# Kernel optimization log

Hardware: AMD Instinct MI355X
Metric: run time of the kernel (lower is better)

## Reference

```python
import jax, jax.numpy as jnp
import numpy as np

NUM_HEADS = 8
LN_EPS = 1e-8


def setup_inputs() -> dict:
    key = jax.random.key(0)
    ks = jax.random.split(key, 10)
    B, Sq, Sk, D, U = 8, 1024, 1024, 512, 512
    s = 1.0 / np.sqrt(D)
    return {
        "queries": jax.random.normal(ks[0], (B, Sq, D), jnp.float32),
        "keys": jax.random.normal(ks[1], (B, Sk, D), jnp.float32),
        "Wq": jax.random.normal(ks[2], (D, U), jnp.float32) * s,
        "bq": jnp.zeros((U,), jnp.float32),
        "Wk": jax.random.normal(ks[3], (D, U), jnp.float32) * s,
        "bk": jnp.zeros((U,), jnp.float32),
        "Wv": jax.random.normal(ks[4], (D, U), jnp.float32) * s,
        "bv": jnp.zeros((U,), jnp.float32),
        "gamma": jnp.ones((U,), jnp.float32),
        "beta": jnp.zeros((U,), jnp.float32),
    }


def reference(queries, keys, Wq, bq, Wk, bk, Wv, bv, gamma, beta):
    H = NUM_HEADS
    B, Sq, _ = queries.shape
    Sk = keys.shape[1]
    U = Wq.shape[1]
    Dh = U // H

    # ReLU-activated Q/K/V projections
    Q = jax.nn.relu(queries @ Wq + bq)   # [B,Sq,U]
    K = jax.nn.relu(keys @ Wk + bk)      # [B,Sk,U]
    V = jax.nn.relu(keys @ Wv + bv)      # [B,Sk,U]

    # split_heads: concat(split(x, H, -1), 0) == head-major [H,B,S,Dh]
    Qh = Q.reshape(B, Sq, H, Dh).transpose(2, 0, 1, 3)
    Kh = K.reshape(B, Sk, H, Dh).transpose(2, 0, 1, 3)
    Vh = V.reshape(B, Sk, H, Dh).transpose(2, 0, 1, 3)

    scores = jnp.einsum('hbqd,hbkd->hbqk', Qh, Kh) / jnp.sqrt(
        jnp.asarray(Dh, scores_dtype := Qh.dtype))
    attn = jax.nn.softmax(scores, axis=-1)

    # post-softmax query mask: zero rows where sum(|q|)==0 ([B,Sq,1] bcast)
    qmask = (jnp.sum(jnp.abs(queries), axis=-1, keepdims=True) > 0)
    attn = attn * qmask.astype(attn.dtype)[None]  # [1,B,Sq,1] -> [H,B,Sq,Sk]

    out = jnp.einsum('hbqk,hbkd->hbqd', attn, Vh)  # [H,B,Sq,Dh]
    # merge_heads: inverse of split_heads
    out = out.transpose(1, 2, 0, 3).reshape(B, Sq, U)

    out = out + queries  # residual

    # LayerNorm over last axis (keras default), eps=1e-8
    mu = jnp.mean(out, axis=-1, keepdims=True)
    var = jnp.mean(jnp.square(out - mu), axis=-1, keepdims=True)
    return gamma * (out - mu) * jax.lax.rsqrt(var + LN_EPS) + beta
```

## Files before the change

kernel.cpp:

```cpp
#include <hip/hip_runtime.h>
#include <stdint.h>

#define ROWS 8192
#define UDIM 512
#define SEQ  1024
#define NH   8
#define DH   64
#define SCALE 0.125f
#define LOG2E 1.44269504f
#define SC_Q (SCALE * LOG2E)

typedef unsigned short u16;
typedef __bf16 bf16_t;
typedef bf16_t bf16x8 __attribute__((ext_vector_type(8)));
typedef float f32x4 __attribute__((ext_vector_type(4)));

__device__ __forceinline__ u16 f2bf(float f) {
    union { float f; uint32_t u; } v; v.f = f;
    uint32_t r = v.u + 0x7FFFu + ((v.u >> 16) & 1u);
    return (u16)(r >> 16);
}

__device__ __forceinline__ uint32_t pk_bf16(float a, float b) {
#if __has_builtin(__builtin_amdgcn_cvt_pk_bf16_f32)
    typedef __bf16 bf16x2_t __attribute__((ext_vector_type(2)));
    bf16x2_t r = __builtin_amdgcn_cvt_pk_bf16_f32(a, b);
    union { bf16x2_t v; uint32_t u; } c; c.v = r;
    return c.u;
#else
    return (uint32_t)f2bf(a) | ((uint32_t)f2bf(b) << 16);
#endif
}

__device__ __forceinline__ void async_ld16(u16* lds, const u16* g) {
    __builtin_amdgcn_global_load_lds((const __attribute__((address_space(1))) void*)g,
                                     (__attribute__((address_space(3))) void*)lds, 16, 0, 0);
}

__global__ void convqk_kernel(const float* __restrict__ q, const float* __restrict__ k,
                              u16* __restrict__ qb, u16* __restrict__ kb) {
    int w = threadIdx.x >> 6, lane = threadIdx.x & 63;
    int row = blockIdx.x * 4 + w;
    const float* src = (blockIdx.y == 0) ? q : k;
    u16* dst = (blockIdx.y == 0) ? qb : kb;
    const float4* s4 = (const float4*)(src + (size_t)row * UDIM);
    ushort4* o4 = (ushort4*)(dst + (size_t)row * UDIM);
    for (int j = 0; j < 2; j++) {
        float4 v = s4[j * 64 + lane];
        ushort4 b;
        b.x = f2bf(v.x); b.y = f2bf(v.y); b.z = f2bf(v.z); b.w = f2bf(v.w);
        o4[j * 64 + lane] = b;
    }
}

__global__ void transposeW_kernel(const float* __restrict__ Wq, const float* __restrict__ Wk,
                                  const float* __restrict__ Wv, u16* __restrict__ Wqt,
                                  u16* __restrict__ Wkt, u16* __restrict__ Wvt) {
    const float* in = (blockIdx.z == 0) ? Wq : (blockIdx.z == 1) ? Wk : Wv;
    u16* out = (blockIdx.z == 0) ? Wqt : (blockIdx.z == 1) ? Wkt : Wvt;
    __shared__ float tile[32][33];
    int k0 = blockIdx.y * 32, n0 = blockIdx.x * 32;
    int tx = threadIdx.x & 31, ty = threadIdx.x >> 5;
    for (int r = ty; r < 32; r += 8)
        tile[r][tx] = in[(size_t)(k0 + r) * UDIM + n0 + tx];
    __syncthreads();
    for (int r = ty; r < 32; r += 8)
        out[(size_t)(n0 + r) * UDIM + k0 + tx] = f2bf(tile[tx][r]);
}

#define CPAD 136
__global__ __launch_bounds__(256, 3) void proj_kernel(
    const u16* __restrict__ qb, const u16* __restrict__ kb,
    const u16* __restrict__ Wqt, const u16* __restrict__ Wkt, const u16* __restrict__ Wvt,
    const float* __restrict__ bq, const float* __restrict__ bk, const float* __restrict__ bv,
    u16* __restrict__ Qp, u16* __restrict__ Kp, u16* __restrict__ Vtp)
{
    const int z = blockIdx.z;
    const u16* A = (z == 0) ? qb : kb;
    const u16* W = (z == 0) ? Wqt : (z == 1) ? Wkt : Wvt;
    const float* bias = (z == 0) ? bq : (z == 1) ? bk : bv;

    __shared__ u16 smem[128 * CPAD];
    u16* c_s = smem;

    const int t = threadIdx.x;
    const int lane = t & 63, w = t >> 6;
    const int quad = lane >> 4, l15 = lane & 15;
    const int m0 = blockIdx.x * 128;
    const int n0 = blockIdx.y * 128;

    const int r0 = t >> 2;
    const int s0 = ((t & 3) ^ ((r0 >> 1) & 3)) * 8;
    const u16* Ag0 = &A[(size_t)(m0 + r0) * 512 + s0];
    const u16* Ag1 = Ag0 + (size_t)64 * 512;
    const u16* Wg0 = &W[(size_t)(n0 + r0) * 512 + s0];
    const u16* Wg1 = Wg0 + (size_t)64 * 512;
    u16* al0[2] = { &smem[0 + t * 8],     &smem[4096 + t * 8] };
    u16* al1[2] = { &smem[0 + (t + 256) * 8], &smem[4096 + (t + 256) * 8] };
    u16* bl0[2] = { &smem[8192 + t * 8],      &smem[12288 + t * 8] };
    u16* bl1[2] = { &smem[8192 + (t + 256) * 8], &smem[12288 + (t + 256) * 8] };

    int aoff[2], boff[8];
    for (int mi = 0; mi < 2; mi++) {
        int row = w * 32 + mi * 16 + l15;
        aoff[mi] = row * 32 + (quad ^ ((row >> 1) & 3)) * 8;
    }
    for (int ni = 0; ni < 8; ni++) {
        int row = ni * 16 + l15;
        boff[ni] = row * 32 + (quad ^ ((row >> 1) & 3)) * 8;
    }

    f32x4 acc[2][8];
    for (int mi = 0; mi < 2; mi++)
        for (int ni = 0; ni < 8; ni++)
            acc[mi][ni] = (f32x4){0.f, 0.f, 0.f, 0.f};

    async_ld16(al0[0], Ag0);  async_ld16(al1[0], Ag1);
    async_ld16(bl0[0], Wg0);  async_ld16(bl1[0], Wg1);
    Ag0 += 32; Ag1 += 32; Wg0 += 32; Wg1 += 32;
    __syncthreads();

    for (int kt = 0; kt < 16; kt++) {
        const int cur = kt & 1, nxt = cur ^ 1;
        if (kt < 15) {
            async_ld16(al0[nxt], Ag0);  async_ld16(al1[nxt], Ag1);
            async_ld16(bl0[nxt], Wg0);  async_ld16(bl1[nxt], Wg1);
            Ag0 += 32; Ag1 += 32; Wg0 += 32; Wg1 += 32;
        }
        const int ab = cur ? 4096 : 0, bb = cur ? 12288 : 8192;
        bf16x8 af[2], bf[8];
        for (int mi = 0; mi < 2; mi++) af[mi] = *(const bf16x8*)&smem[ab + aoff[mi]];
        for (int ni = 0; ni < 8; ni++) bf[ni] = *(const bf16x8*)&smem[bb + boff[ni]];
        for (int mi = 0; mi < 2; mi++)
            for (int ni = 0; ni < 8; ni++)
                acc[mi][ni] = __builtin_amdgcn_mfma_f32_16x16x32_bf16(af[mi], bf[ni], acc[mi][ni], 0, 0, 0);
        __syncthreads();
    }

    const float qscale = (z == 0) ? SC_Q : 1.f;
    float bvl[8];
    for (int ni = 0; ni < 8; ni++) bvl[ni] = bias[n0 + ni * 16 + l15];
    for (int mi = 0; mi < 2; mi++)
        for (int ni = 0; ni < 8; ni++)
            for (int r = 0; r < 4; r++)
                acc[mi][ni][r] = fmaxf(acc[mi][ni][r] + bvl[ni], 0.f) * qscale;

    if (z < 2) {
        for (int mi = 0; mi < 2; mi++)
            for (int ni = 0; ni < 8; ni++)
                for (int r = 0; r < 4; r++)
                    c_s[(w * 32 + mi * 16 + quad * 4 + r) * CPAD + ni * 16 + l15] =
                        f2bf(acc[mi][ni][r]);
        __syncthreads();
        u16* outp = (z == 0) ? Qp : Kp;
        for (int j = 0; j < 8; j++) {
            int c = t + j * 256;
            int mrow = c >> 4, col8 = c & 15;
            uint4 d = *(const uint4*)&c_s[mrow * CPAD + col8 * 8];
            *(uint4*)&outp[(size_t)(m0 + mrow) * 512 + n0 + col8 * 8] = d;
        }
    } else {
        for (int mi = 0; mi < 2; mi++)
            for (int ni = 0; ni < 8; ni++) {
                uint2 pk;
                pk.x = pk_bf16(acc[mi][ni][0], acc[mi][ni][1]);
                pk.y = pk_bf16(acc[mi][ni][2], acc[mi][ni][3]);
                *(uint2*)&c_s[(ni * 16 + l15) * CPAD + w * 32 + mi * 16 + quad * 4] = pk;
            }
        __syncthreads();
        const int bb2 = m0 >> 10, sk0 = m0 & 1023;
        for (int j = 0; j < 8; j++) {
            int c = t + j * 256;
            int nrow = c >> 4, col8 = c & 15;
            uint4 d = *(const uint4*)&c_s[nrow * CPAD + col8 * 8];
            *(uint4*)&Vtp[(size_t)(bb2 * 512 + n0 + nrow) * 1024 + sk0 + col8 * 8] = d;
        }
    }
}

__global__ __launch_bounds__(256, 4) void attn_kernel(
    const u16* __restrict__ Qb, const u16* __restrict__ Kb, const u16* __restrict__ Vt,
    float* __restrict__ O)
{
    __shared__ u16 k_s[2][64 * 64];
    __shared__ u16 v_s[2][64 * 64];
    __shared__ u16 p_s[64 * 64];

    const int t = threadIdx.x, lane = t & 63, w = t >> 6;
    const int quad = lane >> 4, l15 = lane & 15;
    const int fid = blockIdx.x;
    const int xcd = fid & 7, j = fid >> 3;
    const int hb = xcd * 8 + (j & 7);
    const int qt = j >> 3;
    const int h = hb & 7, b = hb >> 3;
    const int q0 = qt * 64;

    const int r0 = t >> 3;
    const int s0 = ((t & 7) ^ (r0 & 7)) * 8;
    const u16* kg0 = &Kb[(size_t)(b * 1024 + r0) * 512 + h * 64 + s0];
    const u16* kg1 = kg0 + (size_t)32 * 512;
    const u16* vg0 = &Vt[(size_t)(b * 512 + h * 64 + r0) * 1024 + s0];
    const u16* vg1 = vg0 + (size_t)32 * 1024;
    u16* kd0[2] = { &k_s[0][t * 8], &k_s[1][t * 8] };
    u16* kd1[2] = { &k_s[0][(t + 256) * 8], &k_s[1][(t + 256) * 8] };
    u16* vd0[2] = { &v_s[0][t * 8], &v_s[1][t * 8] };
    u16* vd1[2] = { &v_s[0][(t + 256) * 8], &v_s[1][(t + 256) * 8] };

    const int prow = w * 16 + l15;
    bf16x8 bqf[2];
    {
        int qrow = b * 1024 + q0 + prow;
        for (int kk = 0; kk < 2; kk++)
            bqf[kk] = *(const bf16x8*)&Qb[(size_t)qrow * 512 + h * 64 + kk * 32 + quad * 8];
    }

    int koff[4][2], pwoff[4], proff[2];
    for (int mi = 0; mi < 4; mi++) {
        int row = mi * 16 + l15;
        koff[mi][0] = row * 64 + (quad ^ (row & 7)) * 8;
        koff[mi][1] = row * 64 + ((4 + quad) ^ (row & 7)) * 8;
    }
    for (int mi = 0; mi < 4; mi++)
        pwoff[mi] = prow * 64 + ((mi * 2 + (quad >> 1)) ^ (prow & 7)) * 8 + (quad & 1) * 4;
    for (int kk = 0; kk < 2; kk++)
        proff[kk] = prow * 64 + ((kk * 4 + quad) ^ (prow & 7)) * 8;

    float l_lane = 0.f;
    f32x4 o_acc[4];
    for (int mi = 0; mi < 4; mi++) o_acc[mi] = (f32x4){0.f, 0.f, 0.f, 0.f};

    async_ld16(kd0[0], kg0);  async_ld16(kd1[0], kg1);
    async_ld16(vd0[0], vg0);  async_ld16(vd1[0], vg1);
    kg0 += (size_t)64 * 512; kg1 += (size_t)64 * 512;
    vg0 += 64; vg1 += 64;
    __syncthreads();

    for (int it = 0; it < 16; it++) {
        const int cur = it & 1, nxt = cur ^ 1;

        if (it < 15) {
            async_ld16(kd0[nxt], kg0);  async_ld16(kd1[nxt], kg1);
            async_ld16(vd0[nxt], vg0);  async_ld16(vd1[nxt], vg1);
            kg0 += (size_t)64 * 512; kg1 += (size_t)64 * 512;
            vg0 += 64; vg1 += 64;
        }

        bf16x8 ak[4][2];
        for (int mi = 0; mi < 4; mi++) {
            ak[mi][0] = *(const bf16x8*)&k_s[cur][koff[mi][0]];
            ak[mi][1] = *(const bf16x8*)&k_s[cur][koff[mi][1]];
        }
        bf16x8 av[2][4];
        for (int kk = 0; kk < 2; kk++)
            for (int mi = 0; mi < 4; mi++)
                av[kk][mi] = *(const bf16x8*)&v_s[cur][koff[mi][kk]];

        f32x4 st[4];
        for (int mi = 0; mi < 4; mi++) {
            f32x4 a = (f32x4){0.f, 0.f, 0.f, 0.f};
            a = __builtin_amdgcn_mfma_f32_16x16x32_bf16(ak[mi][0], bqf[0], a, 0, 0, 0);
            a = __builtin_amdgcn_mfma_f32_16x16x32_bf16(ak[mi][1], bqf[1], a, 0, 0, 0);
            st[mi] = a;
        }
        for (int mi = 0; mi < 4; mi++) {
            float p0 = exp2f(st[mi][0]);
            float p1 = exp2f(st[mi][1]);
            float p2 = exp2f(st[mi][2]);
            float p3 = exp2f(st[mi][3]);
            l_lane += (p0 + p1) + (p2 + p3);
            uint2 pk;
            pk.x = pk_bf16(p0, p1);
            pk.y = pk_bf16(p2, p3);
            *(uint2*)&p_s[pwoff[mi]] = pk;
        }

        __syncthreads();

        for (int kk = 0; kk < 2; kk++) {
            bf16x8 bp = *(const bf16x8*)&p_s[proff[kk]];
            for (int mi = 0; mi < 4; mi++)
                o_acc[mi] = __builtin_amdgcn_mfma_f32_16x16x32_bf16(av[kk][mi], bp, o_acc[mi], 0, 0, 0);
        }

        if (it < 15)
            __syncthreads();
    }

    float l = l_lane;
    l += __shfl_xor(l, 16, 64);
    l += __shfl_xor(l, 32, 64);
    float inv = 1.f / l;
    int gq = q0 + prow;
    for (int mi = 0; mi < 4; mi++) {
        float4 o;
        o.x = o_acc[mi][0] * inv;
        o.y = o_acc[mi][1] * inv;
        o.z = o_acc[mi][2] * inv;
        o.w = o_acc[mi][3] * inv;
        *(float4*)&O[(size_t)(b * 1024 + gq) * 512 + h * 64 + mi * 16 + quad * 4] = o;
    }
}

__global__ void ln_kernel(const float* __restrict__ O, const float* __restrict__ q,
                          const float* __restrict__ gamma, const float* __restrict__ beta,
                          float* __restrict__ out)
{
    int w = threadIdx.x >> 6, lane = threadIdx.x & 63;
    int row = blockIdx.x * 4 + w;
    const float4* O4 = (const float4*)(O + (size_t)row * UDIM);
    const float4* q4 = (const float4*)(q + (size_t)row * UDIM);
    float4* o4 = (float4*)(out + (size_t)row * UDIM);

    float4 qq[2], oo[2];
    float am = 0.f;
    for (int j = 0; j < 2; j++) {
        qq[j] = q4[j * 64 + lane];
        oo[j] = O4[j * 64 + lane];
        am += fabsf(qq[j].x) + fabsf(qq[j].y) + fabsf(qq[j].z) + fabsf(qq[j].w);
    }
    for (int off = 32; off; off >>= 1) am += __shfl_xor(am, off, 64);
    float mask = (am > 0.f) ? 1.f : 0.f;

    float4 x[2];
    float s = 0.f, ss = 0.f;
    for (int j = 0; j < 2; j++) {
        float4 v;
        v.x = oo[j].x * mask + qq[j].x;
        v.y = oo[j].y * mask + qq[j].y;
        v.z = oo[j].z * mask + qq[j].z;
        v.w = oo[j].w * mask + qq[j].w;
        x[j] = v;
        s += v.x + v.y + v.z + v.w;
        ss += v.x * v.x + v.y * v.y + v.z * v.z + v.w * v.w;
    }
    for (int off = 32; off; off >>= 1) {
        s += __shfl_xor(s, off, 64);
        ss += __shfl_xor(ss, off, 64);
    }
    float mu = s * (1.f / 512.f);
    float var = ss * (1.f / 512.f) - mu * mu;
    float rs = rsqrtf(var + 1e-8f);
    for (int j = 0; j < 2; j++) {
        float4 g = ((const float4*)gamma)[j * 64 + lane];
        float4 bb = ((const float4*)beta)[j * 64 + lane];
        float4 v;
        v.x = g.x * (x[j].x - mu) * rs + bb.x;
        v.y = g.y * (x[j].y - mu) * rs + bb.y;
        v.z = g.z * (x[j].z - mu) * rs + bb.z;
        v.w = g.w * (x[j].w - mu) * rs + bb.w;
        o4[j * 64 + lane] = v;
    }
}

extern "C" void kernel_launch(void* const* d_in, const int* in_sizes, int n_in,
                              void* d_out, int out_size, void* d_ws, size_t ws_size,
                              hipStream_t stream)
{
    const float* queries = (const float*)d_in[0];
    const float* keys    = (const float*)d_in[1];
    const float* Wq      = (const float*)d_in[2];
    const float* bq      = (const float*)d_in[3];
    const float* Wk      = (const float*)d_in[4];
    const float* bk      = (const float*)d_in[5];
    const float* Wv      = (const float*)d_in[6];
    const float* bv      = (const float*)d_in[7];
    const float* gamma   = (const float*)d_in[8];
    const float* beta    = (const float*)d_in[9];
    float* out = (float*)d_out;

    char* ws = (char*)d_ws;
    size_t off = 0;
    auto alloc = [&](size_t bytes) {
        void* p = ws + off;
        off += (bytes + 255) & ~(size_t)255;
        return p;
    };
    u16* qb   = (u16*)alloc((size_t)ROWS * UDIM * 2);
    u16* kb   = (u16*)alloc((size_t)ROWS * UDIM * 2);
    u16* Wqt  = (u16*)alloc((size_t)UDIM * UDIM * 2);
    u16* Wkt  = (u16*)alloc((size_t)UDIM * UDIM * 2);
    u16* Wvt  = (u16*)alloc((size_t)UDIM * UDIM * 2);
    u16* Qp   = (u16*)alloc((size_t)ROWS * UDIM * 2);
    u16* Kp   = (u16*)alloc((size_t)ROWS * UDIM * 2);
    u16* Vtp  = (u16*)alloc((size_t)ROWS * UDIM * 2);
    float* Of = (float*)alloc((size_t)ROWS * UDIM * 4);

    convqk_kernel<<<dim3(ROWS / 4, 2), 256, 0, stream>>>(queries, keys, qb, kb);
    transposeW_kernel<<<dim3(16, 16, 3), 256, 0, stream>>>(Wq, Wk, Wv, Wqt, Wkt, Wvt);
    proj_kernel<<<dim3(64, 4, 3), 256, 0, stream>>>(qb, kb, Wqt, Wkt, Wvt, bq, bk, bv, Qp, Kp, Vtp);
    attn_kernel<<<1024, 256, 0, stream>>>(Qp, Kp, Vtp, Of);
    ln_kernel<<<ROWS / 4, 256, 0, stream>>>(Of, queries, gamma, beta, out);
}
```

Measured before the change: 160.5 us.

## Switch attention to 32x32x16 MFMA tiles and emit bf16 attention output

Reworks the attention kernel so each wave computes a 32x32 score and output tile with mfma_f32_32x32x16_bf16 instead of sets of 16x16x32 tiles. Each wave now covers only half of the 64-key block, so the row-sum l is combined across waves through LDS. The normalized output is staged through LDS and written as bf16 rather than fp32, halving the intermediate write and the LayerNorm read. The cost is lower output precision before the residual and LayerNorm, plus extra synchronization in the epilogue.

```diff
diff --git a/kernel.cpp b/kernel.cpp
--- a/kernel.cpp
+++ b/kernel.cpp
@@ -14,11 +14,17 @@
 typedef __bf16 bf16_t;
 typedef bf16_t bf16x8 __attribute__((ext_vector_type(8)));
 typedef float f32x4 __attribute__((ext_vector_type(4)));
+typedef float f32x16 __attribute__((ext_vector_type(16)));
 
 __device__ __forceinline__ u16 f2bf(float f) {
     union { float f; uint32_t u; } v; v.f = f;
     uint32_t r = v.u + 0x7FFFu + ((v.u >> 16) & 1u);
     return (u16)(r >> 16);
+}
+
+__device__ __forceinline__ float bf2f(u16 b) {
+    union { uint32_t u; float f; } v; v.u = ((uint32_t)b) << 16;
+    return v.f;
 }
 
 __device__ __forceinline__ uint32_t pk_bf16(float a, float b) {
@@ -180,14 +186,16 @@
 
 __global__ __launch_bounds__(256, 4) void attn_kernel(
     const u16* __restrict__ Qb, const u16* __restrict__ Kb, const u16* __restrict__ Vt,
-    float* __restrict__ O)
+    u16* __restrict__ Obf)
 {
     __shared__ u16 k_s[2][64 * 64];
     __shared__ u16 v_s[2][64 * 64];
     __shared__ u16 p_s[64 * 64];
 
     const int t = threadIdx.x, lane = t & 63, w = t >> 6;
-    const int quad = lane >> 4, l15 = lane & 15;
+    const int l31 = lane & 31, half = lane >> 5;
+    const int wh = w & 1;
+    const int wq = w >> 1;
     const int fid = blockIdx.x;
     const int xcd = fid & 7, j = fid >> 3;
     const int hb = xcd * 8 + (j & 7);
@@ -206,28 +214,29 @@
     u16* vd0[2] = { &v_s[0][t * 8], &v_s[1][t * 8] };
     u16* vd1[2] = { &v_s[0][(t + 256) * 8], &v_s[1][(t + 256) * 8] };
 
-    const int prow = w * 16 + l15;
-    bf16x8 bqf[2];
+    bf16x8 bqf[4];
     {
-        int qrow = b * 1024 + q0 + prow;
-        for (int kk = 0; kk < 2; kk++)
-            bqf[kk] = *(const bf16x8*)&Qb[(size_t)qrow * 512 + h * 64 + kk * 32 + quad * 8];
-    }
-
-    int koff[4][2], pwoff[4], proff[2];
-    for (int mi = 0; mi < 4; mi++) {
-        int row = mi * 16 + l15;
-        koff[mi][0] = row * 64 + (quad ^ (row & 7)) * 8;
-        koff[mi][1] = row * 64 + ((4 + quad) ^ (row & 7)) * 8;
-    }
-    for (int mi = 0; mi < 4; mi++)
-        pwoff[mi] = prow * 64 + ((mi * 2 + (quad >> 1)) ^ (prow & 7)) * 8 + (quad & 1) * 4;
-    for (int kk = 0; kk < 2; kk++)
-        proff[kk] = prow * 64 + ((kk * 4 + quad) ^ (prow & 7)) * 8;
+        int qrow = b * 1024 + q0 + 32 * wq + l31;
+        for (int tk = 0; tk < 4; tk++)
+            bqf[tk] = *(const bf16x8*)&Qb[(size_t)qrow * 512 + h * 64 + tk * 16 + half * 8];
+    }
+
+    int koff[4];
+    {
+        int row = 32 * wh + l31;
+        for (int tk = 0; tk < 4; tk++)
+            koff[tk] = row * 64 + (((2 * tk + half) ^ (row & 7))) * 8;
+    }
+    const int prow = 32 * wq + l31;
+    int pwoff[4], proff[4];
+    for (int g = 0; g < 4; g++)
+        pwoff[g] = prow * 64 + ((4 * wh + g) ^ (prow & 7)) * 8 + half * 4;
+    for (int tk = 0; tk < 4; tk++)
+        proff[tk] = prow * 64 + ((2 * tk + half) ^ (prow & 7)) * 8;
 
     float l_lane = 0.f;
-    f32x4 o_acc[4];
-    for (int mi = 0; mi < 4; mi++) o_acc[mi] = (f32x4){0.f, 0.f, 0.f, 0.f};
+    f32x16 o_acc = (f32x16){0.f,0.f,0.f,0.f,0.f,0.f,0.f,0.f,
+                            0.f,0.f,0.f,0.f,0.f,0.f,0.f,0.f};
 
     async_ld16(kd0[0], kg0);  async_ld16(kd1[0], kg1);
     async_ld16(vd0[0], vg0);  async_ld16(vd1[0], vg1);
@@ -245,79 +254,86 @@
             vg0 += 64; vg1 += 64;
         }
 
-        bf16x8 ak[4][2];
-        for (int mi = 0; mi < 4; mi++) {
-            ak[mi][0] = *(const bf16x8*)&k_s[cur][koff[mi][0]];
-            ak[mi][1] = *(const bf16x8*)&k_s[cur][koff[mi][1]];
-        }
-        bf16x8 av[2][4];
-        for (int kk = 0; kk < 2; kk++)
-            for (int mi = 0; mi < 4; mi++)
-                av[kk][mi] = *(const bf16x8*)&v_s[cur][koff[mi][kk]];
-
-        f32x4 st[4];
-        for (int mi = 0; mi < 4; mi++) {
-            f32x4 a = (f32x4){0.f, 0.f, 0.f, 0.f};
-            a = __builtin_amdgcn_mfma_f32_16x16x32_bf16(ak[mi][0], bqf[0], a, 0, 0, 0);
-            a = __builtin_amdgcn_mfma_f32_16x16x32_bf16(ak[mi][1], bqf[1], a, 0, 0, 0);
-            st[mi] = a;
-        }
-        for (int mi = 0; mi < 4; mi++) {
-            float p0 = exp2f(st[mi][0]);
-            float p1 = exp2f(st[mi][1]);
-            float p2 = exp2f(st[mi][2]);
-            float p3 = exp2f(st[mi][3]);
+        bf16x8 ak[4], av[4];
+        for (int tk = 0; tk < 4; tk++) {
+            ak[tk] = *(const bf16x8*)&k_s[cur][koff[tk]];
+            av[tk] = *(const bf16x8*)&v_s[cur][koff[tk]];
+        }
+
+        f32x16 st = (f32x16){0.f,0.f,0.f,0.f,0.f,0.f,0.f,0.f,
+                             0.f,0.f,0.f,0.f,0.f,0.f,0.f,0.f};
+        for (int tk = 0; tk < 4; tk++)
+            st = __builtin_amdgcn_mfma_f32_32x32x16_bf16(ak[tk], bqf[tk], st, 0, 0, 0);
+
+        for (int g = 0; g < 4; g++) {
+            float p0 = exp2f(st[4 * g + 0]);
+            float p1 = exp2f(st[4 * g + 1]);
+            float p2 = exp2f(st[4 * g + 2]);
+            float p3 = exp2f(st[4 * g + 3]);
             l_lane += (p0 + p1) + (p2 + p3);
             uint2 pk;
             pk.x = pk_bf16(p0, p1);
             pk.y = pk_bf16(p2, p3);
-            *(uint2*)&p_s[pwoff[mi]] = pk;
+            *(uint2*)&p_s[pwoff[g]] = pk;
         }
 
         __syncthreads();
 
-        for (int kk = 0; kk < 2; kk++) {
-            bf16x8 bp = *(const bf16x8*)&p_s[proff[kk]];
-            for (int mi = 0; mi < 4; mi++)
-                o_acc[mi] = __builtin_amdgcn_mfma_f32_16x16x32_bf16(av[kk][mi], bp, o_acc[mi], 0, 0, 0);
+        for (int tk = 0; tk < 4; tk++) {
+            bf16x8 bp = *(const bf16x8*)&p_s[proff[tk]];
+            o_acc = __builtin_amdgcn_mfma_f32_32x32x16_bf16(av[tk], bp, o_acc, 0, 0, 0);
         }
 
         if (it < 15)
             __syncthreads();
     }
 
-    float l = l_lane;
-    l += __shfl_xor(l, 16, 64);
-    l += __shfl_xor(l, 32, 64);
-    float inv = 1.f / l;
-    int gq = q0 + prow;
-    for (int mi = 0; mi < 4; mi++) {
-        float4 o;
-        o.x = o_acc[mi][0] * inv;
-        o.y = o_acc[mi][1] * inv;
-        o.z = o_acc[mi][2] * inv;
-        o.w = o_acc[mi][3] * inv;
-        *(float4*)&O[(size_t)(b * 1024 + gq) * 512 + h * 64 + mi * 16 + quad * 4] = o;
-    }
-}
-
-__global__ void ln_kernel(const float* __restrict__ O, const float* __restrict__ q,
+    __syncthreads();
+    float l2 = l_lane + __shfl_xor(l_lane, 32, 64);
+    float* lbuf = (float*)&k_s[0][0];
+    if (lane < 32) lbuf[w * 32 + l31] = l2;
+    __syncthreads();
+    float ltot = lbuf[w * 32 + l31] + lbuf[(w ^ 1) * 32 + l31];
+    float inv = 1.f / ltot;
+
+    for (int g = 0; g < 4; g++) {
+        uint2 pk;
+        pk.x = pk_bf16(o_acc[4 * g + 0] * inv, o_acc[4 * g + 1] * inv);
+        pk.y = pk_bf16(o_acc[4 * g + 2] * inv, o_acc[4 * g + 3] * inv);
+        *(uint2*)&p_s[pwoff[g]] = pk;
+    }
+    __syncthreads();
+    for (int rnd = 0; rnd < 2; rnd++) {
+        int c = t + rnd * 256;
+        int row = c >> 3, slot = c & 7;
+        int phys = slot ^ (row & 7);
+        uint4 d4 = *(const uint4*)&p_s[row * 64 + phys * 8];
+        *(uint4*)&Obf[(size_t)(b * 1024 + q0 + row) * 512 + h * 64 + slot * 8] = d4;
+    }
+}
+
+__global__ void ln_kernel(const u16* __restrict__ O, const float* __restrict__ q,
                           const float* __restrict__ gamma, const float* __restrict__ beta,
                           float* __restrict__ out)
 {
     int w = threadIdx.x >> 6, lane = threadIdx.x & 63;
     int row = blockIdx.x * 4 + w;
-    const float4* O4 = (const float4*)(O + (size_t)row * UDIM);
     const float4* q4 = (const float4*)(q + (size_t)row * UDIM);
     float4* o4 = (float4*)(out + (size_t)row * UDIM);
 
-    float4 qq[2], oo[2];
+    float4 qq[2];
     float am = 0.f;
     for (int j = 0; j < 2; j++) {
-        qq[j] = q4[j * 64 + lane];
-        oo[j] = O4[j * 64 + lane];
+        qq[j] = q4[2 * lane + j];
         am += fabsf(qq[j].x) + fabsf(qq[j].y) + fabsf(qq[j].z) + fabsf(qq[j].w);
     }
+    uint4 ov = *(const uint4*)&O[(size_t)row * UDIM + lane * 8];
+    float oo[8];
+    oo[0] = bf2f((u16)(ov.x & 0xFFFF));  oo[1] = bf2f((u16)(ov.x >> 16));
+    oo[2] = bf2f((u16)(ov.y & 0xFFFF));  oo[3] = bf2f((u16)(ov.y >> 16));
+    oo[4] = bf2f((u16)(ov.z & 0xFFFF));  oo[5] = bf2f((u16)(ov.z >> 16));
+    oo[6] = bf2f((u16)(ov.w & 0xFFFF));  oo[7] = bf2f((u16)(ov.w >> 16));
+
     for (int off = 32; off; off >>= 1) am += __shfl_xor(am, off, 64);
     float mask = (am > 0.f) ? 1.f : 0.f;
 
@@ -325,10 +341,10 @@
     float s = 0.f, ss = 0.f;
     for (int j = 0; j < 2; j++) {
         float4 v;
-        v.x = oo[j].x * mask + qq[j].x;
-        v.y = oo[j].y * mask + qq[j].y;
-        v.z = oo[j].z * mask + qq[j].z;
-        v.w = oo[j].w * mask + qq[j].w;
+        v.x = oo[4 * j + 0] * mask + qq[j].x;
+        v.y = oo[4 * j + 1] * mask + qq[j].y;
+        v.z = oo[4 * j + 2] * mask + qq[j].z;
+        v.w = oo[4 * j + 3] * mask + qq[j].w;
         x[j] = v;
         s += v.x + v.y + v.z + v.w;
         ss += v.x * v.x + v.y * v.y + v.z * v.z + v.w * v.w;
@@ -341,14 +357,14 @@
     float var = ss * (1.f / 512.f) - mu * mu;
     float rs = rsqrtf(var + 1e-8f);
     for (int j = 0; j < 2; j++) {
-        float4 g = ((const float4*)gamma)[j * 64 + lane];
-        float4 bb = ((const float4*)beta)[j * 64 + lane];
+        float4 g = ((const float4*)gamma)[2 * lane + j];
+        float4 bb = ((const float4*)beta)[2 * lane + j];
         float4 v;
         v.x = g.x * (x[j].x - mu) * rs + bb.x;
         v.y = g.y * (x[j].y - mu) * rs + bb.y;
         v.z = g.z * (x[j].z - mu) * rs + bb.z;
         v.w = g.w * (x[j].w - mu) * rs + bb.w;
-        o4[j * 64 + lane] = v;
+        o4[2 * lane + j] = v;
     }
 }
 
@@ -383,11 +399,11 @@
     u16* Qp   = (u16*)alloc((size_t)ROWS * UDIM * 2);
     u16* Kp   = (u16*)alloc((size_t)ROWS * UDIM * 2);
     u16* Vtp  = (u16*)alloc((size_t)ROWS * UDIM * 2);
-    float* Of = (float*)alloc((size_t)ROWS * UDIM * 4);
+    u16* Obf  = (u16*)alloc((size_t)ROWS * UDIM * 2);
 
     convqk_kernel<<<dim3(ROWS / 4, 2), 256, 0, stream>>>(queries, keys, qb, kb);
     transposeW_kernel<<<dim3(16, 16, 3), 256, 0, stream>>>(Wq, Wk, Wv, Wqt, Wkt, Wvt);
     proj_kernel<<<dim3(64, 4, 3), 256, 0, stream>>>(qb, kb, Wqt, Wkt, Wvt, bq, bk, bv, Qp, Kp, Vtp);
-    attn_kernel<<<1024, 256, 0, stream>>>(Qp, Kp, Vtp, Of);
-    ln_kernel<<<ROWS / 4, 256, 0, stream>>>(Of, queries, gamma, beta, out);
-}
+    attn_kernel<<<1024, 256, 0, stream>>>(Qp, Kp, Vtp, Obf);
+    ln_kernel<<<ROWS / 4, 256, 0, stream>>>(Obf, queries, gamma, beta, out);
+}
```

Result: no change. 161.3 us (+0.5%).
